# Kernel tuning notes

Measured on AMD Instinct MI355X. Metric: run time of the kernel, lower is better.

The kernel has to match this reference:

```python
import jax, jax.numpy as jnp
import numpy as np

N_QUBITS = 8
DIM = 1 << N_QUBITS  # 256 basis states


def _cnot_chain_perm(n):
    # Compose CNOT(0,1)..CNOT(n-2,n-1), CNOT(n-1,0) as a single basis permutation.
    # Convention: wire 0 is the most-significant bit of the basis index.
    idx = np.arange(1 << n)
    f = idx.copy()
    pairs = [(w, w + 1) for w in range(n - 1)] + [(n - 1, 0)]
    for c, t in pairs:
        ctrl = (f >> (n - 1 - c)) & 1
        f = np.where(ctrl == 1, f ^ (1 << (n - 1 - t)), f)
    finv = np.empty_like(f)
    finv[f] = idx  # new_state = old_state[finv]
    return finv

_PERM = jnp.asarray(_cnot_chain_perm(N_QUBITS))
# sign[s, i] = +1 if bit i of basis state s is 0 else -1 (PauliZ eigenvalue)
_SIGN = jnp.asarray(
    1.0 - 2.0 * (((np.arange(DIM)[:, None] >> (N_QUBITS - 1 - np.arange(N_QUBITS))[None, :]) & 1)),
    dtype=np.float32,
)


def _qgate(x, theta):
    """Simulated circuit: RX(x_i) encoder + trainable RX(theta_i) + CNOT ring + <Z_i>.
    RX(x)RX(theta) = RX(x+theta); each qubit amplitude is cos or -i*sin, so basis
    probabilities are real products of cos^2/sin^2, permuted by the CNOT chain.
    x: (B, n) angles, theta: (n,). Returns (B, n) Pauli-Z expectations."""
    alpha = 0.5 * (x + theta)
    p = jnp.stack([jnp.cos(alpha) ** 2, jnp.sin(alpha) ** 2], axis=-1)  # (B, n, 2)
    probs = p[:, 0]  # (B, 2)
    for i in range(1, N_QUBITS):  # outer product over wires -> (B, 2^n)
        probs = (probs[:, :, None] * p[:, i][:, None, :]).reshape(probs.shape[0], -1)
    probs = probs[:, _PERM]  # apply CNOT ring (pure basis permutation)
    return probs @ _SIGN


def setup_inputs() -> dict:
    key = jax.random.key(0)
    ks = jax.random.split(key, 8)
    T, B, D, H, Q = 256, 512, 256, 256, N_QUBITS
    s = lambda k, shape, scale: jax.random.normal(k, shape, jnp.float32) * scale
    return {
        "inputs": jax.random.normal(ks[0], (T, B, D), jnp.float32),
        "W_proj": s(ks[1], (D + H, 4 * Q), 0.05),
        "b_proj": jnp.zeros((4 * Q,), jnp.float32),
        "theta_gate": s(ks[2], (Q,), 1.0),
        "W_qproj": s(ks[3], (Q, H), 0.3),
        "b_qproj": jnp.zeros((H,), jnp.float32),
        "theta_attn": s(ks[4], (Q,), 1.0),
        "W_attn_proj": s(ks[5], (H, Q), 0.05),
        "b_attn_proj": jnp.zeros((Q,), jnp.float32),
        "W_attn_back": s(ks[6], (Q, H), 0.3),
        "b_attn_back": jnp.zeros((H,), jnp.float32),
    }


def reference(inputs, W_proj, b_proj, theta_gate, W_qproj, b_qproj,
              theta_attn, W_attn_proj, b_attn_proj, W_attn_back, b_attn_back):
    T, B, _ = inputs.shape
    H = W_qproj.shape[1]
    hx0 = jnp.zeros((B, H), inputs.dtype)
    cx0 = jnp.zeros((B, H), inputs.dtype)

    def step(carry, x):
        hx, cx = carry
        gates = jnp.concatenate([x, hx], axis=1) @ W_proj + b_proj  # (B, 4*Q)
        f_in, i_in, g_in, o_in = jnp.split(gates, 4, axis=1)
        qp = lambda z: _qgate(z, theta_gate) @ W_qproj + b_qproj
        f = jax.nn.sigmoid(qp(f_in))
        i = jax.nn.sigmoid(qp(i_in))
        g = jnp.tanh(qp(g_in))
        o = jax.nn.sigmoid(qp(o_in))
        cx = f * cx + i * g
        hx = o * jnp.tanh(cx)
        hq = _qgate(hx @ W_attn_proj + b_attn_proj, theta_attn)  # quantum attention
        hx = hq @ W_attn_back + b_attn_back
        return (hx, cx), hx

    (hx, cx), outs = jax.lax.scan(step, (hx0, cx0), inputs)
    return outs, (hx, cx)
```

## Files before the change

kernel.cpp:

```cpp
#include <hip/hip_runtime.h>

#define T_STEPS 256
#define BATCH   512
#define DIN     256
#define HDIM    256

typedef unsigned int u32;
typedef _Float16 h2 __attribute__((ext_vector_type(2)));

__device__ __forceinline__ u32 pack2(float a, float b) {
    return __builtin_bit_cast(u32, __builtin_amdgcn_cvt_pkrtz(a, b));
}
__device__ __forceinline__ float dot2(u32 a, u32 b, float acc) {
    return __builtin_amdgcn_fdot2(__builtin_bit_cast(h2, a),
                                  __builtin_bit_cast(h2, b), acc, false);
}
__device__ __forceinline__ float rcpf(float x) { return __builtin_amdgcn_rcpf(x); }
__device__ __forceinline__ float fast_sigmoid(float x) {
    return rcpf(1.0f + __expf(-x));
}
__device__ __forceinline__ float fast_tanh(float x) {
    return 1.0f - 2.0f * rcpf(__expf(2.0f * x) + 1.0f);
}

template<int CTRL>
__device__ __forceinline__ float dppf(float x) {
    int xi = __builtin_bit_cast(int, x);
    return __builtin_bit_cast(float,
        __builtin_amdgcn_update_dpp(xi, xi, CTRL, 0xF, 0xF, false));
}
#define DPP_XOR1  0xB1
#define DPP_XOR2  0x4E
#define DPP_HMIR  0x141
#define DPP_SHR1  0x111
#define DPP_SHR2  0x112
#define DPP_SHR4  0x114
#define DPP_SHL1  0x101

__device__ __forceinline__ void lds_barrier() {
    asm volatile("s_waitcnt lgkmcnt(0)\n\ts_barrier" ::: "memory");
}

__launch_bounds__(256, 1)
__global__ void xproj_kernel(const float* __restrict__ x,
                             const float* __restrict__ W_proj,
                             const float* __restrict__ b_proj,
                             const float* __restrict__ theta_gate,
                             float* __restrict__ xp) {
    const int tid   = threadIdx.x;
    const int g     = tid & 31;
    const int rs    = tid >> 5;
    const int rows0 = blockIdx.x * 64;
    __shared__ __align__(16) u32 xs[64 * 128];

    u32 Wc[128];
    #pragma unroll
    for (int i = 0; i < 128; ++i)
        Wc[i] = pack2(W_proj[(2 * i) * 32 + g], W_proj[(2 * i + 1) * 32 + g]);
    const float bias = b_proj[g] + theta_gate[g & 7];

    {
        const int r  = tid >> 2;
        const int c0 = (tid & 3) * 8;
        const float* xr = x + (size_t)(rows0 + r) * DIN + c0 * 8;
        #pragma unroll
        for (int w = 0; w < 8; ++w) {
            float4 a = ((const float4*)xr)[2 * w];
            float4 b = ((const float4*)xr)[2 * w + 1];
            uint4 pk = make_uint4(pack2(a.x, a.y), pack2(a.z, a.w),
                                  pack2(b.x, b.y), pack2(b.z, b.w));
            *(uint4*)&xs[r * 128 + ((c0 + w) ^ (r & 7)) * 4] = pk;
        }
    }
    __syncthreads();

    #pragma unroll 1
    for (int it = 0; it < 8; ++it) {
        const int row = it * 8 + rs;
        const u32* xrow = &xs[row * 128];
        const int sw = row & 7;
        float a0 = 0.f, a1 = 0.f, a2 = 0.f, a3 = 0.f;
        #pragma unroll
        for (int c = 0; c < 32; c += 4) {
            uint4 v0 = *(const uint4*)&xrow[((c + 0) ^ sw) * 4];
            uint4 v1 = *(const uint4*)&xrow[((c + 1) ^ sw) * 4];
            uint4 v2 = *(const uint4*)&xrow[((c + 2) ^ sw) * 4];
            uint4 v3 = *(const uint4*)&xrow[((c + 3) ^ sw) * 4];
            a0 = dot2(v0.x, Wc[(c+0)*4+0], a0); a0 = dot2(v0.y, Wc[(c+0)*4+1], a0);
            a0 = dot2(v0.z, Wc[(c+0)*4+2], a0); a0 = dot2(v0.w, Wc[(c+0)*4+3], a0);
            a1 = dot2(v1.x, Wc[(c+1)*4+0], a1); a1 = dot2(v1.y, Wc[(c+1)*4+1], a1);
            a1 = dot2(v1.z, Wc[(c+1)*4+2], a1); a1 = dot2(v1.w, Wc[(c+1)*4+3], a1);
            a2 = dot2(v2.x, Wc[(c+2)*4+0], a2); a2 = dot2(v2.y, Wc[(c+2)*4+1], a2);
            a2 = dot2(v2.z, Wc[(c+2)*4+2], a2); a2 = dot2(v2.w, Wc[(c+2)*4+3], a2);
            a3 = dot2(v3.x, Wc[(c+3)*4+0], a3); a3 = dot2(v3.y, Wc[(c+3)*4+1], a3);
            a3 = dot2(v3.z, Wc[(c+3)*4+2], a3); a3 = dot2(v3.w, Wc[(c+3)*4+3], a3);
        }
        xp[(size_t)(rows0 + row) * 32 + g] = (a0 + a1) + (a2 + a3) + bias;
    }
}

__launch_bounds__(256, 2)
__global__ void qlstm_main(const float* __restrict__ xp_all,
                           const float* __restrict__ W_proj,
                           const float* __restrict__ W_qproj,
                           const float* __restrict__ b_qproj,
                           const float* __restrict__ theta_attn,
                           const float* __restrict__ W_attn_proj,
                           const float* __restrict__ b_attn_proj,
                           const float* __restrict__ W_attn_back,
                           const float* __restrict__ b_attn_back,
                           float* __restrict__ out) {
    const int tid  = threadIdx.x;
    const int b    = blockIdx.x;
    const int w    = tid >> 6;
    const int lw   = tid & 63;
    const int g    = lw & 31;
    const int q    = lw & 7;
    const int o    = lw >> 3;

    __shared__ __align__(16) u32 hS[128];
    __shared__ __align__(16) u32 hmS[160];
    __shared__ __align__(16) u32 ogS[64];
    __shared__ __align__(16) float caS[32];
    __shared__ __align__(16) float preS[128];

    u32 WhP[16];
    {
        const int dbase = DIN + 64 * w + (lw >> 5) * 32;
        #pragma unroll
        for (int i = 0; i < 16; ++i)
            WhP[i] = pack2(W_proj[(dbase + 2 * i) * 32 + g],
                           W_proj[(dbase + 2 * i + 1) * 32 + g]);
    }
    u32 WqpP[4];
    #pragma unroll
    for (int p = 0; p < 4; ++p)
        WqpP[p] = pack2(W_qproj[(2 * p) * HDIM + tid],
                        W_qproj[(2 * p + 1) * HDIM + tid]);
    u32 WapP[16];
    #pragma unroll
    for (int i = 0; i < 16; ++i)
        WapP[i] = pack2(W_attn_proj[(32 * q + 2 * i) * 8 + o],
                        W_attn_proj[(32 * q + 2 * i + 1) * 8 + o]);
    u32 WabP[4];
    #pragma unroll
    for (int p = 0; p < 4; ++p)
        WabP[p] = pack2(W_attn_back[(2 * p) * HDIM + tid],
                        W_attn_back[(2 * p + 1) * HDIM + tid]);
    const float bqp = b_qproj[tid];
    const float bap = b_attn_proj[o] + theta_attn[o];
    const float bab = b_attn_back[tid];

    if (tid < 128) hS[tid] = 0u;
    float cx = 0.f, hx = 0.f;
    float xpc = xp_all[(size_t)b * 32 + g];
    __syncthreads();

    for (int t = 0; t < T_STEPS; ++t) {
        float xpn = 0.f;
        if (t + 1 < T_STEPS)
            xpn = xp_all[((size_t)(t + 1) * BATCH + b) * 32 + b == b ? ((size_t)(t + 1) * BATCH + b) * 32 + g - (((size_t)(t + 1) * BATCH + b) * 32) : 0];
        if (t + 1 < T_STEPS)
            xpn = xp_all[((size_t)(t + 1) * BATCH + b) * 32 + g];

        const int hbase = 32 * w + (lw >> 5) * 16;
        const uint4* hp = (const uint4*)&hS[hbase];
        uint4 v0 = hp[0], v1 = hp[1], v2 = hp[2], v3 = hp[3];
        float a0 = dot2(v0.x, WhP[ 0], 0.f);
        a0 = dot2(v0.y, WhP[ 1], a0);
        a0 = dot2(v0.z, WhP[ 2], a0);
        a0 = dot2(v0.w, WhP[ 3], a0);
        float a1 = dot2(v1.x, WhP[ 4], 0.f);
        a1 = dot2(v1.y, WhP[ 5], a1);
        a1 = dot2(v1.z, WhP[ 6], a1);
        a1 = dot2(v1.w, WhP[ 7], a1);
        float a2 = dot2(v2.x, WhP[ 8], 0.f);
        a2 = dot2(v2.y, WhP[ 9], a2);
        a2 = dot2(v2.z, WhP[10], a2);
        a2 = dot2(v2.w, WhP[11], a2);
        float a3 = dot2(v3.x, WhP[12], 0.f);
        a3 = dot2(v3.y, WhP[13], a3);
        a3 = dot2(v3.z, WhP[14], a3);
        a3 = dot2(v3.w, WhP[15], a3);
        float part = (a0 + a1) + (a2 + a3);
        part += __shfl_xor(part, 32);
        if (lw < 32) preS[w * 32 + lw] = part;
        lds_barrier();
        float pre = ((preS[g] + preS[32 + g]) + (preS[64 + g] + preS[96 + g])) + xpc;
        float cq = __cosf(pre);

        float s = cq;
        { float u1 = dppf<DPP_SHR1>(s); if (q >= 1) s *= u1; }
        { float u2 = dppf<DPP_SHR2>(s); if (q >= 2) s *= u2; }
        { float u4 = dppf<DPP_SHR4>(s); if (q >= 4) s *= u4; }
        float v = (q == 0) ? 1.0f : cq;
        v *= dppf<DPP_XOR1>(v);
        v *= dppf<DPP_XOR2>(v);
        v *= dppf<DPP_HMIR>(v);
        float outv = (q == 0) ? v : s;
        float onx  = dppf<DPP_SHL1>(outv);
        if (lw < 32 && !(lw & 1))
            ogS[w * 16 + (lw >> 1)] = pack2(outv, onx);

        const uint4* ogp = (const uint4*)&ogS[w * 16];
        uint4 og0 = ogp[0], og1 = ogp[1], og2 = ogp[2], og3 = ogp[3];
        float d0 = dot2(og0.x, WqpP[0], bqp);
        d0 = dot2(og0.y, WqpP[1], d0);
        d0 = dot2(og0.z, WqpP[2], d0);
        d0 = dot2(og0.w, WqpP[3], d0);
        float d1 = dot2(og1.x, WqpP[0], bqp);
        d1 = dot2(og1.y, WqpP[1], d1);
        d1 = dot2(og1.z, WqpP[2], d1);
        d1 = dot2(og1.w, WqpP[3], d1);
        float d2 = dot2(og2.x, WqpP[0], bqp);
        d2 = dot2(og2.y, WqpP[1], d2);
        d2 = dot2(og2.z, WqpP[2], d2);
        d2 = dot2(og2.w, WqpP[3], d2);
        float d3 = dot2(og3.x, WqpP[0], bqp);
        d3 = dot2(og3.y, WqpP[1], d3);
        d3 = dot2(og3.z, WqpP[2], d3);
        d3 = dot2(og3.w, WqpP[3], d3);
        float fv = fast_sigmoid(d0);
        float iv = fast_sigmoid(d1);
        float gv = fast_tanh(d2);
        float ov = fast_sigmoid(d3);
        cx = fmaf(fv, cx, iv * gv);
        float hm = ov * fast_tanh(cx);
        float hmn = dppf<DPP_SHL1>(hm);
        if (!(tid & 1))
            hmS[(tid >> 5) * 20 + ((tid >> 1) & 15)] = pack2(hm, hmn);
        lds_barrier();

        const uint4* mp = (const uint4*)&hmS[q * 20];
        uint4 m0 = mp[0], m1 = mp[1], m2 = mp[2], m3 = mp[3];
        float s0 = dot2(m0.x, WapP[ 0], 0.f);
        s0 = dot2(m0.y, WapP[ 1], s0);
        s0 = dot2(m0.z, WapP[ 2], s0);
        s0 = dot2(m0.w, WapP[ 3], s0);
        float s1 = dot2(m1.x, WapP[ 4], 0.f);
        s1 = dot2(m1.y, WapP[ 5], s1);
        s1 = dot2(m1.z, WapP[ 6], s1);
        s1 = dot2(m1.w, WapP[ 7], s1);
        float s2 = dot2(m2.x, WapP[ 8], 0.f);
        s2 = dot2(m2.y, WapP[ 9], s2);
        s2 = dot2(m2.z, WapP[10], s2);
        s2 = dot2(m2.w, WapP[11], s2);
        float s3 = dot2(m3.x, WapP[12], 0.f);
        s3 = dot2(m3.y, WapP[13], s3);
        s3 = dot2(m3.z, WapP[14], s3);
        s3 = dot2(m3.w, WapP[15], s3);
        float sd = (s0 + s1) + (s2 + s3);
        sd += dppf<DPP_XOR1>(sd);
        sd += dppf<DPP_XOR2>(sd);
        sd += dppf<DPP_HMIR>(sd);
        float co = __cosf(sd + bap);
        if (!(lw & 7)) caS[w * 8 + o] = co;

        float4 cA = *(const float4*)&caS[w * 8];
        float4 cB = *(const float4*)&caS[w * 8 + 4];
        float p1 = cA.x * cA.y;
        float p2 = p1 * cA.z;
        float p3 = p2 * cA.w;
        float p4 = p3 * cB.x;
        float p5 = p4 * cB.y;
        float p6 = p5 * cB.z;
        float p7 = p6 * cB.w;
        float q12 = cA.y * cA.z, q34 = cA.w * cB.x, q56 = cB.y * cB.z;
        float p0 = (q12 * q34) * (q56 * cB.w);
        u32 oq0 = pack2(p0, p1);
        u32 oq1 = pack2(p2, p3);
        u32 oq2 = pack2(p4, p5);
        u32 oq3 = pack2(p6, p7);
        float hv = dot2(oq0, WabP[0], bab);
        hv = dot2(oq1, WabP[1], hv);
        hv = dot2(oq2, WabP[2], hv);
        hv = dot2(oq3, WabP[3], hv);
        hx = hv;
        out[((size_t)t * BATCH + b) * HDIM + tid] = hx;
        float hxn = dppf<DPP_SHL1>(hx);
        if (!(tid & 1))
            hS[tid >> 1] = pack2(hx, hxn);
        xpc = xpn;
        lds_barrier();
    }

    const size_t base = (size_t)T_STEPS * BATCH * HDIM;
    out[base + (size_t)b * HDIM + tid] = hx;
    out[base + (size_t)BATCH * HDIM + (size_t)b * HDIM + tid] = cx;
}

extern "C" void kernel_launch(void* const* d_in, const int* in_sizes, int n_in,
                              void* d_out, int out_size, void* d_ws, size_t ws_size,
                              hipStream_t stream) {
    const float* inputs      = (const float*)d_in[0];
    const float* W_proj      = (const float*)d_in[1];
    const float* b_proj      = (const float*)d_in[2];
    const float* theta_gate  = (const float*)d_in[3];
    const float* W_qproj     = (const float*)d_in[4];
    const float* b_qproj     = (const float*)d_in[5];
    const float* theta_attn  = (const float*)d_in[6];
    const float* W_attn_proj = (const float*)d_in[7];
    const float* b_attn_proj = (const float*)d_in[8];
    const float* W_attn_back = (const float*)d_in[9];
    const float* b_attn_back = (const float*)d_in[10];
    float* outp = (float*)d_out;
    float* xp   = (float*)d_ws;

    xproj_kernel<<<(T_STEPS * BATCH) / 64, 256, 0, stream>>>(
        inputs, W_proj, b_proj, theta_gate, xp);
    qlstm_main<<<BATCH, 256, 0, stream>>>(
        xp, W_proj, W_qproj, b_qproj, theta_attn,
        W_attn_proj, b_attn_proj, W_attn_back, b_attn_back, outp);
}
```

Baseline: 340.5 us.

## Fuse input projection into recurrent kernel with double-buffered x staging

Removes the separate input-projection kernel and computes x@W_proj inside the recurrent loop. Each step prefetches the next timestep's input row from global memory and stages it as packed fp16 in a double-buffered LDS slot. This drops one kernel launch and the workspace round-trip for the projected gates. In exchange the per-step critical path doubles its dot2 work, and each step now loads 256 floats instead of 32.

```diff
diff --git a/kernel.cpp b/kernel.cpp
--- a/kernel.cpp
+++ b/kernel.cpp
@@ -41,75 +41,19 @@
     asm volatile("s_waitcnt lgkmcnt(0)\n\ts_barrier" ::: "memory");
 }
 
-__launch_bounds__(256, 1)
-__global__ void xproj_kernel(const float* __restrict__ x,
-                             const float* __restrict__ W_proj,
-                             const float* __restrict__ b_proj,
-                             const float* __restrict__ theta_gate,
-                             float* __restrict__ xp) {
-    const int tid   = threadIdx.x;
-    const int g     = tid & 31;
-    const int rs    = tid >> 5;
-    const int rows0 = blockIdx.x * 64;
-    __shared__ __align__(16) u32 xs[64 * 128];
-
-    u32 Wc[128];
-    #pragma unroll
-    for (int i = 0; i < 128; ++i)
-        Wc[i] = pack2(W_proj[(2 * i) * 32 + g], W_proj[(2 * i + 1) * 32 + g]);
-    const float bias = b_proj[g] + theta_gate[g & 7];
-
-    {
-        const int r  = tid >> 2;
-        const int c0 = (tid & 3) * 8;
-        const float* xr = x + (size_t)(rows0 + r) * DIN + c0 * 8;
-        #pragma unroll
-        for (int w = 0; w < 8; ++w) {
-            float4 a = ((const float4*)xr)[2 * w];
-            float4 b = ((const float4*)xr)[2 * w + 1];
-            uint4 pk = make_uint4(pack2(a.x, a.y), pack2(a.z, a.w),
-                                  pack2(b.x, b.y), pack2(b.z, b.w));
-            *(uint4*)&xs[r * 128 + ((c0 + w) ^ (r & 7)) * 4] = pk;
-        }
-    }
-    __syncthreads();
-
-    #pragma unroll 1
-    for (int it = 0; it < 8; ++it) {
-        const int row = it * 8 + rs;
-        const u32* xrow = &xs[row * 128];
-        const int sw = row & 7;
-        float a0 = 0.f, a1 = 0.f, a2 = 0.f, a3 = 0.f;
-        #pragma unroll
-        for (int c = 0; c < 32; c += 4) {
-            uint4 v0 = *(const uint4*)&xrow[((c + 0) ^ sw) * 4];
-            uint4 v1 = *(const uint4*)&xrow[((c + 1) ^ sw) * 4];
-            uint4 v2 = *(const uint4*)&xrow[((c + 2) ^ sw) * 4];
-            uint4 v3 = *(const uint4*)&xrow[((c + 3) ^ sw) * 4];
-            a0 = dot2(v0.x, Wc[(c+0)*4+0], a0); a0 = dot2(v0.y, Wc[(c+0)*4+1], a0);
-            a0 = dot2(v0.z, Wc[(c+0)*4+2], a0); a0 = dot2(v0.w, Wc[(c+0)*4+3], a0);
-            a1 = dot2(v1.x, Wc[(c+1)*4+0], a1); a1 = dot2(v1.y, Wc[(c+1)*4+1], a1);
-            a1 = dot2(v1.z, Wc[(c+1)*4+2], a1); a1 = dot2(v1.w, Wc[(c+1)*4+3], a1);
-            a2 = dot2(v2.x, Wc[(c+2)*4+0], a2); a2 = dot2(v2.y, Wc[(c+2)*4+1], a2);
-            a2 = dot2(v2.z, Wc[(c+2)*4+2], a2); a2 = dot2(v2.w, Wc[(c+2)*4+3], a2);
-            a3 = dot2(v3.x, Wc[(c+3)*4+0], a3); a3 = dot2(v3.y, Wc[(c+3)*4+1], a3);
-            a3 = dot2(v3.z, Wc[(c+3)*4+2], a3); a3 = dot2(v3.w, Wc[(c+3)*4+3], a3);
-        }
-        xp[(size_t)(rows0 + row) * 32 + g] = (a0 + a1) + (a2 + a3) + bias;
-    }
-}
-
 __launch_bounds__(256, 2)
-__global__ void qlstm_main(const float* __restrict__ xp_all,
-                           const float* __restrict__ W_proj,
-                           const float* __restrict__ W_qproj,
-                           const float* __restrict__ b_qproj,
-                           const float* __restrict__ theta_attn,
-                           const float* __restrict__ W_attn_proj,
-                           const float* __restrict__ b_attn_proj,
-                           const float* __restrict__ W_attn_back,
-                           const float* __restrict__ b_attn_back,
-                           float* __restrict__ out) {
+__global__ void qlstm_fused(const float* __restrict__ inputs,
+                            const float* __restrict__ W_proj,
+                            const float* __restrict__ b_proj,
+                            const float* __restrict__ theta_gate,
+                            const float* __restrict__ W_qproj,
+                            const float* __restrict__ b_qproj,
+                            const float* __restrict__ theta_attn,
+                            const float* __restrict__ W_attn_proj,
+                            const float* __restrict__ b_attn_proj,
+                            const float* __restrict__ W_attn_back,
+                            const float* __restrict__ b_attn_back,
+                            float* __restrict__ out) {
     const int tid  = threadIdx.x;
     const int b    = blockIdx.x;
     const int w    = tid >> 6;
@@ -119,18 +63,22 @@
     const int o    = lw >> 3;
 
     __shared__ __align__(16) u32 hS[128];
+    __shared__ __align__(16) u32 xS[256];
     __shared__ __align__(16) u32 hmS[160];
     __shared__ __align__(16) u32 ogS[64];
     __shared__ __align__(16) float caS[32];
     __shared__ __align__(16) float preS[128];
 
-    u32 WhP[16];
+    u32 WxP[16], WhP[16];
     {
-        const int dbase = DIN + 64 * w + (lw >> 5) * 32;
+        const int dbase = 64 * w + (lw >> 5) * 32;
         #pragma unroll
-        for (int i = 0; i < 16; ++i)
-            WhP[i] = pack2(W_proj[(dbase + 2 * i) * 32 + g],
+        for (int i = 0; i < 16; ++i) {
+            WxP[i] = pack2(W_proj[(dbase + 2 * i) * 32 + g],
                            W_proj[(dbase + 2 * i + 1) * 32 + g]);
+            WhP[i] = pack2(W_proj[(DIN + dbase + 2 * i) * 32 + g],
+                           W_proj[(DIN + dbase + 2 * i + 1) * 32 + g]);
+        }
     }
     u32 WqpP[4];
     #pragma unroll
@@ -147,38 +95,60 @@
     for (int p = 0; p < 4; ++p)
         WabP[p] = pack2(W_attn_back[(2 * p) * HDIM + tid],
                         W_attn_back[(2 * p + 1) * HDIM + tid]);
-    const float bqp = b_qproj[tid];
-    const float bap = b_attn_proj[o] + theta_attn[o];
-    const float bab = b_attn_back[tid];
+    const float bqp  = b_qproj[tid];
+    const float bap  = b_attn_proj[o] + theta_attn[o];
+    const float bab  = b_attn_back[tid];
+    const float bias = b_proj[g] + theta_gate[g & 7];
 
     if (tid < 128) hS[tid] = 0u;
+    {
+        float x0  = inputs[(size_t)b * DIN + tid];
+        float x0n = dppf<DPP_SHL1>(x0);
+        if (!(tid & 1)) xS[tid >> 1] = pack2(x0, x0n);
+    }
     float cx = 0.f, hx = 0.f;
-    float xpc = xp_all[(size_t)b * 32 + g];
     __syncthreads();
 
     for (int t = 0; t < T_STEPS; ++t) {
-        float xpn = 0.f;
+        const int xb = (t & 1) << 7;
+        float xn = 0.f;
         if (t + 1 < T_STEPS)
-            xpn = xp_all[((size_t)(t + 1) * BATCH + b) * 32 + b == b ? ((size_t)(t + 1) * BATCH + b) * 32 + g - (((size_t)(t + 1) * BATCH + b) * 32) : 0];
-        if (t + 1 < T_STEPS)
-            xpn = xp_all[((size_t)(t + 1) * BATCH + b) * 32 + g];
-
-        const int hbase = 32 * w + (lw >> 5) * 16;
-        const uint4* hp = (const uint4*)&hS[hbase];
+            xn = inputs[((size_t)(t + 1) * BATCH + b) * DIN + tid];
+
+        const int sbase = 32 * w + (lw >> 5) * 16;
+        const uint4* xp = (const uint4*)&xS[xb + sbase];
+        const uint4* hp = (const uint4*)&hS[sbase];
+        uint4 x0 = xp[0], x1 = xp[1], x2 = xp[2], x3 = xp[3];
         uint4 v0 = hp[0], v1 = hp[1], v2 = hp[2], v3 = hp[3];
-        float a0 = dot2(v0.x, WhP[ 0], 0.f);
+        float a0 = dot2(x0.x, WxP[ 0], 0.f);
+        a0 = dot2(x0.y, WxP[ 1], a0);
+        a0 = dot2(x0.z, WxP[ 2], a0);
+        a0 = dot2(x0.w, WxP[ 3], a0);
+        float a1 = dot2(x1.x, WxP[ 4], 0.f);
+        a1 = dot2(x1.y, WxP[ 5], a1);
+        a1 = dot2(x1.z, WxP[ 6], a1);
+        a1 = dot2(x1.w, WxP[ 7], a1);
+        float a2 = dot2(x2.x, WxP[ 8], 0.f);
+        a2 = dot2(x2.y, WxP[ 9], a2);
+        a2 = dot2(x2.z, WxP[10], a2);
+        a2 = dot2(x2.w, WxP[11], a2);
+        float a3 = dot2(x3.x, WxP[12], 0.f);
+        a3 = dot2(x3.y, WxP[13], a3);
+        a3 = dot2(x3.z, WxP[14], a3);
+        a3 = dot2(x3.w, WxP[15], a3);
+        a0 = dot2(v0.x, WhP[ 0], a0);
         a0 = dot2(v0.y, WhP[ 1], a0);
         a0 = dot2(v0.z, WhP[ 2], a0);
         a0 = dot2(v0.w, WhP[ 3], a0);
-        float a1 = dot2(v1.x, WhP[ 4], 0.f);
+        a1 = dot2(v1.x, WhP[ 4], a1);
         a1 = dot2(v1.y, WhP[ 5], a1);
         a1 = dot2(v1.z, WhP[ 6], a1);
         a1 = dot2(v1.w, WhP[ 7], a1);
-        float a2 = dot2(v2.x, WhP[ 8], 0.f);
+        a2 = dot2(v2.x, WhP[ 8], a2);
         a2 = dot2(v2.y, WhP[ 9], a2);
         a2 = dot2(v2.z, WhP[10], a2);
         a2 = dot2(v2.w, WhP[11], a2);
-        float a3 = dot2(v3.x, WhP[12], 0.f);
+        a3 = dot2(v3.x, WhP[12], a3);
         a3 = dot2(v3.y, WhP[13], a3);
         a3 = dot2(v3.z, WhP[14], a3);
         a3 = dot2(v3.w, WhP[15], a3);
@@ -186,7 +156,7 @@
         part += __shfl_xor(part, 32);
         if (lw < 32) preS[w * 32 + lw] = part;
         lds_barrier();
-        float pre = ((preS[g] + preS[32 + g]) + (preS[64 + g] + preS[96 + g])) + xpc;
+        float pre = ((preS[g] + preS[32 + g]) + (preS[64 + g] + preS[96 + g])) + bias;
         float cq = __cosf(pre);
 
         float s = cq;
@@ -280,7 +250,10 @@
         float hxn = dppf<DPP_SHL1>(hx);
         if (!(tid & 1))
             hS[tid >> 1] = pack2(hx, hxn);
-        xpc = xpn;
+        {
+            float xnx = dppf<DPP_SHL1>(xn);
+            if (!(tid & 1)) xS[(xb ^ 128) + (tid >> 1)] = pack2(xn, xnx);
+        }
         lds_barrier();
     }
 
@@ -304,11 +277,8 @@
     const float* W_attn_back = (const float*)d_in[9];
     const float* b_attn_back = (const float*)d_in[10];
     float* outp = (float*)d_out;
-    float* xp   = (float*)d_ws;
-
-    xproj_kernel<<<(T_STEPS * BATCH) / 64, 256, 0, stream>>>(
-        inputs, W_proj, b_proj, theta_gate, xp);
-    qlstm_main<<<BATCH, 256, 0, stream>>>(
-        xp, W_proj, W_qproj, b_qproj, theta_attn,
+
+    qlstm_fused<<<BATCH, 256, 0, stream>>>(
+        inputs, W_proj, b_proj, theta_gate, W_qproj, b_qproj, theta_attn,
         W_attn_proj, b_attn_proj, W_attn_back, b_attn_back, outp);
 }
```

Measured after the change: 301.7 us. 1.13x faster.
